# Performance work log

Hardware: AMD Instinct MI355X
Metric: run time of the kernel (lower is better)

The kernel has to match this reference:

```python
import jax, jax.numpy as jnp
import numpy as np

B, S = 8, 192
MAX_ITER = 3


def setup_inputs() -> dict:
    key = jax.random.key(0)
    k1, k2 = jax.random.split(key)
    s_con = jax.random.normal(k1, (B, S, S), dtype=jnp.float32)
    s_bin = jax.random.normal(k2, (B, S, S, S), dtype=jnp.float32)
    mask = jnp.ones((B, S, S), dtype=bool)
    return {"s_con": s_con, "s_bin": s_bin, "mask": mask}


def reference(s_con, s_bin, mask):
    # Faithful port of MFVIConstituency.mfvi, kept in batch-first layout.
    # Torch code permutes to [i, j, (k,) b]; math is identical with b leading.
    S_ = s_con.shape[-1]
    idx = jnp.arange(S_)
    # mask2o[b,i,j,k] = mask[b,i,j] & (i != k) & (j != k)
    ne_i = idx[:, None, None] != idx[None, None, :]   # [S,1,S]
    ne_j = idx[None, :, None] != idx[None, None, :]   # [1,S,S]
    mask2o = mask[:, :, :, None] & ne_i[None] & ne_j[None]  # [B,S,S,S]
    sb = s_bin * mask2o
    # fixed-point iterations: q[b,i,j] = s_con[b,i,j] + sum_k sigmoid(q)[b,j,k] * sb[b,i,j,k]
    q = s_con
    for _ in range(MAX_ITER):
        q = s_con + jnp.einsum('bjk,bijk->bij', jax.nn.sigmoid(q), sb)
    return jax.nn.sigmoid(q)
```

## Files before the change

kernel.cpp:

```cpp
#include <hip/hip_runtime.h>


#define S_DIM 192
#define SS (S_DIM * S_DIM)
#define B_DIM 8
#define NROWS (B_DIM * SS)

typedef float    floatx4 __attribute__((ext_vector_type(4)));
typedef _Float16 halfx4  __attribute__((ext_vector_type(4)));

__device__ __forceinline__ float sigmoidf(float x) {
    return 1.0f / (1.0f + __expf(-x));
}

__global__ __launch_bounds__(256) void fvi_first_kernel(const float* __restrict__ s_con,
                                                        const float* __restrict__ s_bin,
                                                        const int* __restrict__ mask,
                                                        halfx4* __restrict__ sbh,
                                                        float* __restrict__ sig_out) {
    const int wave = threadIdx.x >> 6;
    const int lane = threadIdx.x & 63;
    const int grp  = lane >> 4;
    const int sub  = lane & 15;
    const int row  = (blockIdx.x * 4 + wave) * 4 + grp;

    const int b   = row / SS;
    const int rem = row - b * SS;
    const int i   = rem / S_DIM;
    const int j   = rem - i * S_DIM;

    const floatx4* __restrict__ srow = reinterpret_cast<const floatx4*>(s_bin + (size_t)row * S_DIM);
    const float4*  __restrict__ grow = reinterpret_cast<const float4*>(s_con + (size_t)(b * SS + j * S_DIM));
    halfx4* __restrict__ hrow = sbh + (size_t)row * (S_DIM / 4);

    float dot = 0.0f;
    #pragma unroll
    for (int c = 0; c < 3; ++c) {
        const int f4 = sub + (c << 4);
        floatx4 sv = __builtin_nontemporal_load(srow + f4);
        float4  gv = grow[f4];
        const int k0 = f4 << 2;
        const float m0 = (k0 + 0 != i && k0 + 0 != j) ? sv.x : 0.0f;
        const float m1 = (k0 + 1 != i && k0 + 1 != j) ? sv.y : 0.0f;
        const float m2 = (k0 + 2 != i && k0 + 2 != j) ? sv.z : 0.0f;
        const float m3 = (k0 + 3 != i && k0 + 3 != j) ? sv.w : 0.0f;
        dot += m0 * sigmoidf(gv.x) + m1 * sigmoidf(gv.y)
             + m2 * sigmoidf(gv.z) + m3 * sigmoidf(gv.w);
        halfx4 hv;
        hv.x = (_Float16)m0; hv.y = (_Float16)m1;
        hv.z = (_Float16)m2; hv.w = (_Float16)m3;
        __builtin_nontemporal_store(hv, hrow + f4);
    }

    dot += __shfl_xor(dot, 1, 64);
    dot += __shfl_xor(dot, 2, 64);
    dot += __shfl_xor(dot, 4, 64);
    dot += __shfl_xor(dot, 8, 64);

    if (sub == 0) {
        float q = s_con[row] + (mask[row] ? dot : 0.0f);
        sig_out[row] = sigmoidf(q);
    }
}

__global__ __launch_bounds__(256) void fvi_iter_kernel(const float* __restrict__ s_con,
                                                       const halfx4* __restrict__ sbh,
                                                       const int* __restrict__ mask,
                                                       const float* __restrict__ sig_in,
                                                       float* __restrict__ sig_out) {
    const int wave = threadIdx.x >> 6;
    const int lane = threadIdx.x & 63;
    const int grp  = lane >> 4;
    const int sub  = lane & 15;
    const int row  = (blockIdx.x * 4 + wave) * 4 + grp;

    const int b   = row / SS;
    const int rem = row - b * SS;
    const int j   = rem - (rem / S_DIM) * S_DIM;

    const halfx4* __restrict__ hrow = sbh + (size_t)row * (S_DIM / 4);
    const float4* __restrict__ grow = reinterpret_cast<const float4*>(sig_in + (size_t)(b * SS + j * S_DIM));

    float dot = 0.0f;
    #pragma unroll
    for (int c = 0; c < 3; ++c) {
        const int f4 = sub + (c << 4);
        halfx4 hv = __builtin_nontemporal_load(hrow + f4);
        float4 gv = grow[f4];
        dot += (float)hv.x * gv.x + (float)hv.y * gv.y
             + (float)hv.z * gv.z + (float)hv.w * gv.w;
    }

    dot += __shfl_xor(dot, 1, 64);
    dot += __shfl_xor(dot, 2, 64);
    dot += __shfl_xor(dot, 4, 64);
    dot += __shfl_xor(dot, 8, 64);

    if (sub == 0) {
        float q = s_con[row] + (mask[row] ? dot : 0.0f);
        sig_out[row] = sigmoidf(q);
    }
}

extern "C" void kernel_launch(void* const* d_in, const int* in_sizes, int n_in,
                              void* d_out, int out_size, void* d_ws, size_t ws_size,
                              hipStream_t stream) {
    const float* s_con = (const float*)d_in[0];
    const float* s_bin = (const float*)d_in[1];
    const int*   mask  = (const int*)d_in[2];
    float* out  = (float*)d_out;
    float* sigA = (float*)d_ws;
    float* sigB = sigA + NROWS;
    halfx4* sbh = reinterpret_cast<halfx4*>(sigB + NROWS);

    const dim3 grid(NROWS / 16);

    fvi_first_kernel<<<grid, 256, 0, stream>>>(s_con, s_bin, mask, sbh, sigA);
    fvi_iter_kernel <<<grid, 256, 0, stream>>>(s_con, sbh, mask, sigA, sigB);
    fvi_iter_kernel <<<grid, 256, 0, stream>>>(s_con, sbh, mask, sigB, out);
}
```

Measured before the change: 118.7 us.

## Precompute fp16 sigmoid, store sigmoid state in fp16, widen iter loads to 16B

```diff
diff --git a/kernel.cpp b/kernel.cpp
--- a/kernel.cpp
+++ b/kernel.cpp
@@ -8,16 +8,30 @@
 
 typedef float    floatx4 __attribute__((ext_vector_type(4)));
 typedef _Float16 halfx4  __attribute__((ext_vector_type(4)));
+typedef _Float16 halfx8  __attribute__((ext_vector_type(8)));
 
 __device__ __forceinline__ float sigmoidf(float x) {
     return 1.0f / (1.0f + __expf(-x));
 }
 
+__global__ __launch_bounds__(256) void sig0_kernel(const float* __restrict__ s_con,
+                                                   _Float16* __restrict__ sigh0) {
+    const int idx = (blockIdx.x * 256 + threadIdx.x) * 4;
+    floatx4 v = *reinterpret_cast<const floatx4*>(s_con + idx);
+    halfx4 h;
+    h.x = (_Float16)sigmoidf(v.x);
+    h.y = (_Float16)sigmoidf(v.y);
+    h.z = (_Float16)sigmoidf(v.z);
+    h.w = (_Float16)sigmoidf(v.w);
+    *reinterpret_cast<halfx4*>(sigh0 + idx) = h;
+}
+
 __global__ __launch_bounds__(256) void fvi_first_kernel(const float* __restrict__ s_con,
                                                         const float* __restrict__ s_bin,
                                                         const int* __restrict__ mask,
-                                                        halfx4* __restrict__ sbh,
-                                                        float* __restrict__ sig_out) {
+                                                        const _Float16* __restrict__ sigh0,
+                                                        halfx8* __restrict__ sbh8,
+                                                        _Float16* __restrict__ sigh_out) {
     const int wave = threadIdx.x >> 6;
     const int lane = threadIdx.x & 63;
     const int grp  = lane >> 4;
@@ -30,26 +44,31 @@
     const int j   = rem - i * S_DIM;
 
     const floatx4* __restrict__ srow = reinterpret_cast<const floatx4*>(s_bin + (size_t)row * S_DIM);
-    const float4*  __restrict__ grow = reinterpret_cast<const float4*>(s_con + (size_t)(b * SS + j * S_DIM));
-    halfx4* __restrict__ hrow = sbh + (size_t)row * (S_DIM / 4);
+    const halfx4*  __restrict__ grow = reinterpret_cast<const halfx4*>(sigh0 + (size_t)(b * SS + j * S_DIM));
+    halfx8* __restrict__ hrow = sbh8 + (size_t)row * (S_DIM / 8);
 
     float dot = 0.0f;
     #pragma unroll
     for (int c = 0; c < 3; ++c) {
         const int f4 = sub + (c << 4);
         floatx4 sv = __builtin_nontemporal_load(srow + f4);
-        float4  gv = grow[f4];
+        halfx4  gv = grow[f4];
         const int k0 = f4 << 2;
         const float m0 = (k0 + 0 != i && k0 + 0 != j) ? sv.x : 0.0f;
         const float m1 = (k0 + 1 != i && k0 + 1 != j) ? sv.y : 0.0f;
         const float m2 = (k0 + 2 != i && k0 + 2 != j) ? sv.z : 0.0f;
         const float m3 = (k0 + 3 != i && k0 + 3 != j) ? sv.w : 0.0f;
-        dot += m0 * sigmoidf(gv.x) + m1 * sigmoidf(gv.y)
-             + m2 * sigmoidf(gv.z) + m3 * sigmoidf(gv.w);
+        dot += m0 * (float)gv.x + m1 * (float)gv.y + m2 * (float)gv.z + m3 * (float)gv.w;
         halfx4 hv;
         hv.x = (_Float16)m0; hv.y = (_Float16)m1;
         hv.z = (_Float16)m2; hv.w = (_Float16)m3;
-        __builtin_nontemporal_store(hv, hrow + f4);
+        int2 hb = __builtin_bit_cast(int2, hv);
+        int px = __shfl_down(hb.x, 1, 64);
+        int py = __shfl_down(hb.y, 1, 64);
+        if (!(sub & 1)) {
+            int4 w4 = { hb.x, hb.y, px, py };
+            hrow[f4 >> 1] = __builtin_bit_cast(halfx8, w4);
+        }
     }
 
     dot += __shfl_xor(dot, 1, 64);
@@ -59,46 +78,50 @@
 
     if (sub == 0) {
         float q = s_con[row] + (mask[row] ? dot : 0.0f);
-        sig_out[row] = sigmoidf(q);
+        sigh_out[row] = (_Float16)sigmoidf(q);
     }
 }
 
+template <bool LAST>
 __global__ __launch_bounds__(256) void fvi_iter_kernel(const float* __restrict__ s_con,
-                                                       const halfx4* __restrict__ sbh,
+                                                       const halfx8* __restrict__ sbh8,
                                                        const int* __restrict__ mask,
-                                                       const float* __restrict__ sig_in,
-                                                       float* __restrict__ sig_out) {
+                                                       const _Float16* __restrict__ sigh_in,
+                                                       _Float16* __restrict__ sigh_out,
+                                                       float* __restrict__ out32) {
     const int wave = threadIdx.x >> 6;
     const int lane = threadIdx.x & 63;
-    const int grp  = lane >> 4;
-    const int sub  = lane & 15;
-    const int row  = (blockIdx.x * 4 + wave) * 4 + grp;
+    const int grp  = lane >> 3;
+    const int sub  = lane & 7;
+    const int row  = (blockIdx.x * 4 + wave) * 8 + grp;
 
     const int b   = row / SS;
     const int rem = row - b * SS;
     const int j   = rem - (rem / S_DIM) * S_DIM;
 
-    const halfx4* __restrict__ hrow = sbh + (size_t)row * (S_DIM / 4);
-    const float4* __restrict__ grow = reinterpret_cast<const float4*>(sig_in + (size_t)(b * SS + j * S_DIM));
+    const halfx8* __restrict__ hrow = sbh8 + (size_t)row * (S_DIM / 8);
+    const halfx8* __restrict__ grow = reinterpret_cast<const halfx8*>(sigh_in + (size_t)(b * SS + j * S_DIM));
 
     float dot = 0.0f;
     #pragma unroll
     for (int c = 0; c < 3; ++c) {
-        const int f4 = sub + (c << 4);
-        halfx4 hv = __builtin_nontemporal_load(hrow + f4);
-        float4 gv = grow[f4];
-        dot += (float)hv.x * gv.x + (float)hv.y * gv.y
-             + (float)hv.z * gv.z + (float)hv.w * gv.w;
+        const int f8 = sub + (c << 3);
+        halfx8 h = hrow[f8];
+        halfx8 g = grow[f8];
+        dot += (float)h[0] * (float)g[0] + (float)h[1] * (float)g[1]
+             + (float)h[2] * (float)g[2] + (float)h[3] * (float)g[3]
+             + (float)h[4] * (float)g[4] + (float)h[5] * (float)g[5]
+             + (float)h[6] * (float)g[6] + (float)h[7] * (float)g[7];
     }
 
     dot += __shfl_xor(dot, 1, 64);
     dot += __shfl_xor(dot, 2, 64);
     dot += __shfl_xor(dot, 4, 64);
-    dot += __shfl_xor(dot, 8, 64);
 
     if (sub == 0) {
         float q = s_con[row] + (mask[row] ? dot : 0.0f);
-        sig_out[row] = sigmoidf(q);
+        float s = sigmoidf(q);
+        if (LAST) out32[row] = s; else sigh_out[row] = (_Float16)s;
     }
 }
 
@@ -108,14 +131,15 @@
     const float* s_con = (const float*)d_in[0];
     const float* s_bin = (const float*)d_in[1];
     const int*   mask  = (const int*)d_in[2];
-    float* out  = (float*)d_out;
-    float* sigA = (float*)d_ws;
-    float* sigB = sigA + NROWS;
-    halfx4* sbh = reinterpret_cast<halfx4*>(sigB + NROWS);
+    float* out = (float*)d_out;
 
-    const dim3 grid(NROWS / 16);
+    _Float16* sigh0 = (_Float16*)d_ws;
+    _Float16* sighA = sigh0 + NROWS;
+    _Float16* sighB = sighA + NROWS;
+    halfx8*   sbh8  = reinterpret_cast<halfx8*>(sighB + NROWS);
 
-    fvi_first_kernel<<<grid, 256, 0, stream>>>(s_con, s_bin, mask, sbh, sigA);
-    fvi_iter_kernel <<<grid, 256, 0, stream>>>(s_con, sbh, mask, sigA, sigB);
-    fvi_iter_kernel <<<grid, 256, 0, stream>>>(s_con, sbh, mask, sigB, out);
+    sig0_kernel<<<NROWS / 1024, 256, 0, stream>>>(s_con, sigh0);
+    fvi_first_kernel<<<NROWS / 16, 256, 0, stream>>>(s_con, s_bin, mask, sigh0, sbh8, sighA);
+    fvi_iter_kernel<false><<<NROWS / 32, 256, 0, stream>>>(s_con, sbh8, mask, sighA, sighB, nullptr);
+    fvi_iter_kernel<true ><<<NROWS / 32, 256, 0, stream>>>(s_con, sbh8, mask, sighB, nullptr, out);
 }
```

Result: faster. 100.0 us (-15.7%).
